# Kernel optimization log

Measured on AMD Instinct MI355X. Metric: run time of the kernel, lower is better.

Reference implementation:

```python
import jax, jax.numpy as jnp
import numpy as np

B = 8; DIM = 384; H = 8; DH = 48; T = 256; T2 = 64; DEPTH = 4; P = 14; G = 16
SCALE = DIM ** -0.5
BN_INV = 1.0 / float(np.sqrt(1.0 + 1e-5))

def _gelu(x):
    return jax.nn.gelu(x, approximate=False)

def _ln(x, g, b):
    m = x.mean(-1, keepdims=True)
    v = ((x - m) ** 2).mean(-1, keepdims=True)
    return (x - m) / jnp.sqrt(v + 1e-5) * g + b

def _conv(x, w, bi, s, p, groups=1):
    y = jax.lax.conv_general_dilated(x, w, (s, s), [(p, p), (p, p)],
        dimension_numbers=('NCHW', 'OIHW', 'NCHW'), feature_group_count=groups)
    return y + bi[None, :, None, None]

def _gumbel_softmax(logits, key, tau=1.0):
    g = jax.random.gumbel(key, logits.shape, logits.dtype)
    return jax.nn.softmax((logits + g) / tau, axis=-1)

def setup_inputs() -> dict:
    key = jax.random.key(0)
    ks = jax.random.split(key, 20)
    def n(k, shape, s=0.02):
        return jax.random.normal(k, shape, jnp.float32) * s
    D = DEPTH
    return {
        'img': jax.random.normal(ks[0], (B, 3, 224, 224), jnp.float32),
        'adj': jax.random.randint(ks[1], (T, T), 0, 2).astype(jnp.int32),
        'ln_g': jnp.ones((D, DIM), jnp.float32), 'ln_b': jnp.zeros((D, DIM), jnp.float32),
        'gcn_wq': n(ks[2], (D, DH, DH)), 'gcn_wk': n(ks[3], (D, DH, DH)), 'gcn_wv': n(ks[4], (D, DH, DH)),
        'wq': n(ks[5], (D, DIM, DIM)), 'wk': n(ks[6], (D, DIM, DIM)), 'wv': n(ks[7], (D, DIM, DIM)),
        'w_kf': n(ks[8], (D, 2 * DIM, H)), 'w_kf2': n(ks[9], (D, H, T)), 'w_kf3': n(ks[10], (D, H, T2)),
        'sD': jnp.ones((D, H, T), jnp.float32), 'sD2': jnp.ones((D, H, T2), jnp.float32),
        'randmat': n(ks[11], (D, H, H), 1.0),
        'conv1_w': n(ks[12], (DIM, 3, 3, 3), 0.05), 'conv1_b': jnp.zeros((DIM,), jnp.float32),
        'bn_g': jnp.ones((DIM,), jnp.float32), 'bn_b': jnp.zeros((DIM,), jnp.float32),
        'conv2_w': n(ks[13], (DIM, 1, 3, 3), 0.05), 'conv2_b': jnp.zeros((DIM,), jnp.float32),
        'emb_w': n(ks[14], (4 * DIM, DIM)), 'emb_b': jnp.zeros((DIM,), jnp.float32),
        'upool_w': n(ks[15], (DIM, T2)), 'upool_b': jnp.zeros((T2,), jnp.float32),
        'upoolout_w': n(ks[16], (DIM, 1)), 'upoolout_b': jnp.zeros((1,), jnp.float32),
    }

def _forward(img, adj, ln_g, ln_b, gcn_wq, gcn_wk, gcn_wv, wq, wk, wv,
             w_kf, w_kf2, w_kf3, sD, sD2, randmat,
             conv1_w, conv1_b, bn_g, bn_b, conv2_w, conv2_b, emb_w, emb_b,
             upool_w, upool_b, upoolout_w, upoolout_b):
    b = img.shape[0]
    # patchify: (b,3,224,224) -> (b*256, 3, 14, 14)
    x = img.reshape(b, 3, G, P, G, P).transpose(0, 2, 4, 1, 3, 5).reshape(b * G * G, 3, P, P)
    y = _conv(x, conv1_w, conv1_b, 2, 1)                       # (b*256,384,7,7)
    y = y * BN_INV * bn_g[None, :, None, None] + bn_b[None, :, None, None]  # BN eval (mean=0,var=1)
    y = _gelu(y)
    y = _conv(y, conv2_w, conv2_b, 2, 1, groups=DIM)           # depthwise -> (b*256,384,4,4)
    y = y.reshape(b * G * G, DIM, 2, 2, 2, 2).max(axis=(3, 5)) # adaptive max pool -> 2x2
    y = y.reshape(b, G * G, DIM * 4)                           # (b,256, c*p1*p2)
    x = y @ emb_w + emb_b                                      # (b,256,384)
    rep_adj = jnp.broadcast_to(adj.astype(jnp.float32)[None, None], (b, H, T, T))

    def attention(xn, adjbh, i, label):
        t = xn.shape[1]
        x4 = xn.reshape(b, t, H, DH).transpose(0, 2, 1, 3)     # b h t d
        q4 = jnp.einsum('bhts,bhsd->bhtd', adjbh, x4 @ gcn_wq[i])  # GCN: A @ (X W)
        k4 = jnp.einsum('bhts,bhsd->bhtd', adjbh, x4 @ gcn_wk[i])
        q = q4.transpose(0, 2, 1, 3).reshape(b, t, DIM) @ wq[i]
        k = k4.transpose(0, 2, 1, 3).reshape(b, t, DIM) @ wk[i]
        rm0 = _gelu(jnp.concatenate([q, k], -1) @ w_kf[i])     # (b,t,h)
        rm = jnp.einsum('bth,btg->bhg', rm0, rm0)
        if label == 0:
            rmd = jax.nn.sigmoid((rm @ w_kf2[i]) / sD[i])      # (b,h,t)
        else:
            rmd = jax.nn.sigmoid((rm @ w_kf3[i]) / sD2[i])
        qh = q.reshape(b, t, H, DH).transpose(0, 2, 1, 3)
        kh = k.reshape(b, t, H, DH).transpose(0, 2, 1, 3)
        score = jnp.einsum('bhld,bhtd->bhlt', qh, kh) * SCALE
        score = jax.nn.leaky_relu(score)
        score = rmd[:, :, :, None] * score * rmd[:, :, None, :]   # diag_embed(rmd) @ S @ diag_embed(rmd)
        score = jnp.einsum('lh,bhk->blk', randmat[i], score.reshape(b, H, t * t)).reshape(b, H, t, t)
        score = jnp.where(adjbh > 0, score, -1e12)
        attn = jax.nn.softmax(score, axis=-1)
        v4 = jnp.einsum('bhts,bhsd->bhtd', attn, x4 @ gcn_wv[i])  # attn weights as edge weights
        return _gelu(v4.transpose(0, 2, 1, 3).reshape(b, t, DIM) @ wv[i])

    kg = jax.random.key(42)
    for i in range(DEPTH):
        xn = _ln(x, ln_g[i], ln_b[i])
        if i < DEPTH // 2:
            x = attention(xn, rep_adj, i, 0) + x
        else:
            if i == DEPTH // 2:
                tmp = (x @ upool_w + upool_b).transpose(0, 2, 1)       # (b,64,256)
                tmp = _gumbel_softmax(tmp, jax.random.fold_in(kg, i))
                x = tmp @ x                                            # (b,64,384)
                rep_adj = jnp.einsum('bls,bhst->bhlt', tmp, rep_adj)   # C A C^T
                rep_adj = jnp.einsum('bhlt,bmt->bhlm', rep_adj, tmp)
                xn = _ln(x, ln_g[i], ln_b[i])
            x = attention(xn, rep_adj, i, 1) + x

    tmp = (x @ upoolout_w + upoolout_b).transpose(0, 2, 1)             # (b,1,64)
    tmp = _gumbel_softmax(tmp, jax.random.fold_in(kg, 99))
    return tmp @ x                                                     # (b,1,384)

def reference(img, adj, ln_g, ln_b, gcn_wq, gcn_wk, gcn_wv, wq, wk, wv,
              w_kf, w_kf2, w_kf3, sD, sD2, randmat,
              conv1_w, conv1_b, bn_g, bn_b, conv2_w, conv2_b, emb_w, emb_b,
              upool_w, upool_b, upoolout_w, upoolout_b):
    return _forward(img, adj, ln_g, ln_b, gcn_wq, gcn_wk, gcn_wv, wq, wk, wv,
                    w_kf, w_kf2, w_kf3, sD, sD2, randmat,
                    conv1_w, conv1_b, bn_g, bn_b, conv2_w, conv2_b, emb_w, emb_b,
                    upool_w, upool_b, upoolout_w, upoolout_b)
```

## Files before the change

### kernel.cpp

```cpp
#include <hip/hip_runtime.h>
#include <stdint.h>
#include <math.h>

#define NB 8
#define NDIM 384
#define NHD 8
#define DHD 48

__device__ float g_patch[2048 * 1536];
__device__ float g_x[NB * 256 * NDIM];
__device__ float g_xb[NB * 64 * NDIM];
__device__ float g_xq[NB * NHD * 256 * DHD];
__device__ float g_xk[NB * NHD * 256 * DHD];
__device__ float g_xv[NB * NHD * 256 * DHD];
__device__ float g_q4[NB * 256 * NDIM];
__device__ float g_k4[NB * 256 * NDIM];
__device__ float g_q[NB * 256 * NDIM];
__device__ float g_k[NB * 256 * NDIM];
__device__ float g_rm0[NB * 256 * NHD];
__device__ float g_rm[NB * 64];
__device__ float g_rmd[NB * NHD * 256];
__device__ float g_score[NB * NHD * 256 * 256];
__device__ float g_score2[NB * NHD * 256 * 256];
__device__ float g_logits[NB * 256 * 64];
__device__ float g_tmp[NB * 64 * 256];
__device__ float g_e1[NB * 64 * 256];
__device__ float g_adj2[NB * 64 * 64];
__device__ float g_lg2[NB * 64];

__device__ __forceinline__ float* dev_buf(int s) {
  switch (s) {
    case 0: return g_patch;
    case 1: return g_x;
    case 2: return g_q4;
    case 3: return g_k4;
    case 4: return g_q;
    case 5: return g_k;
    case 6: return g_logits;
    default: return nullptr;
  }
}
#define SEL_PATCH 0
#define SEL_X 1
#define SEL_Q4 2
#define SEL_K4 3
#define SEL_Q 4
#define SEL_K 5
#define SEL_LOGITS 6

__device__ __forceinline__ float gelu_f(float x) {
  return 0.5f * x * (1.0f + erff(x * 0.70710678118654752440f));
}

__host__ __device__ inline void threefry2x32(uint32_t k0, uint32_t k1,
                                             uint32_t x0, uint32_t x1,
                                             uint32_t* o0, uint32_t* o1) {
  uint32_t ks2 = k0 ^ k1 ^ 0x1BD11BDAu;
#define TF_R(r) { x0 += x1; x1 = (x1 << (r)) | (x1 >> (32 - (r))); x1 ^= x0; }
  x0 += k0; x1 += k1;
  TF_R(13) TF_R(15) TF_R(26) TF_R(6)
  x0 += k1; x1 += ks2 + 1u;
  TF_R(17) TF_R(29) TF_R(16) TF_R(24)
  x0 += ks2; x1 += k0 + 2u;
  TF_R(13) TF_R(15) TF_R(26) TF_R(6)
  x0 += k0; x1 += k1 + 3u;
  TF_R(17) TF_R(29) TF_R(16) TF_R(24)
  x0 += k1; x1 += ks2 + 4u;
  TF_R(13) TF_R(15) TF_R(26) TF_R(6)
  x0 += ks2; x1 += k0 + 5u;
#undef TF_R
  *o0 = x0; *o1 = x1;
}

__device__ __forceinline__ double gumbel_from(uint32_t k0, uint32_t k1,
                                              uint32_t idx) {
  uint32_t o0, o1;
  threefry2x32(k0, k1, 0u, idx, &o0, &o1);
  uint32_t bits = o0 ^ o1;
  uint32_t ub = (bits >> 9) | 0x3f800000u;
  float f = __uint_as_float(ub) - 1.0f;
  const float tiny = 1.17549435e-38f;
  float u = fmaxf(f + tiny, tiny);
  return -log(-log((double)u));
}

__global__ __launch_bounds__(256) void k_patch(const float* __restrict__ img,
                                               const float* __restrict__ w1, const float* __restrict__ b1,
                                               const float* __restrict__ bng, const float* __restrict__ bnb,
                                               const float* __restrict__ w2, const float* __restrict__ b2) {
  __shared__ float s_in[3 * 16 * 16];
  __shared__ float s_c1[96 * 49];
  __shared__ float s_w1[96 * 27];
  const float BN_INV = (float)0.99999500003749968752;
  int p = blockIdx.x;
  int b = p >> 8, g = p & 255, gi = g >> 4, gj = g & 15;
  int tid = threadIdx.x;
  for (int i = tid; i < 3 * 256; i += 256) s_in[i] = 0.f;
  __syncthreads();
  for (int idx = tid; idx < 3 * 196; idx += 256) {
    int c = idx / 196, r = idx % 196, py = r / 14, px = r % 14;
    s_in[c * 256 + (py + 1) * 16 + (px + 1)] =
        img[(((size_t)b * 3 + c) * 224 + gi * 14 + py) * 224 + gj * 14 + px];
  }
  __syncthreads();
  int wave = tid >> 6, lane = tid & 63;
  int y = lane / 7, x = lane - y * 7;
  bool act = lane < 49;
  float in[27];
#pragma unroll
  for (int c = 0; c < 3; ++c)
#pragma unroll
    for (int ky = 0; ky < 3; ++ky)
#pragma unroll
      for (int kx = 0; kx < 3; ++kx)
        in[c * 9 + ky * 3 + kx] = act ? s_in[c * 256 + (2 * y + ky) * 16 + (2 * x + kx)] : 0.f;

  for (int chunk = 0; chunk < 4; ++chunk) {
    int obase = chunk * 96;
    const float4* wsrc = (const float4*)(w1 + obase * 27);
    for (int i = tid; i < 96 * 27 / 4; i += 256) ((float4*)s_w1)[i] = wsrc[i];
    __syncthreads();
    for (int ci = 0; ci < 24; ci += 4) {
      int cl0 = wave * 24 + ci;
      int o0 = obase + cl0;
      float a0 = b1[o0], a1 = b1[o0 + 1], a2 = b1[o0 + 2], a3 = b1[o0 + 3];
      const float* wA = s_w1 + cl0 * 27;
#pragma unroll
      for (int j = 0; j < 27; ++j) {
        float ij = in[j];
        a0 += ij * wA[j];
        a1 += ij * wA[27 + j];
        a2 += ij * wA[54 + j];
        a3 += ij * wA[81 + j];
      }
      a0 = a0 * BN_INV * bng[o0] + bnb[o0];
      a1 = a1 * BN_INV * bng[o0 + 1] + bnb[o0 + 1];
      a2 = a2 * BN_INV * bng[o0 + 2] + bnb[o0 + 2];
      a3 = a3 * BN_INV * bng[o0 + 3] + bnb[o0 + 3];
      if (act) {
        s_c1[cl0 * 49 + lane] = gelu_f(a0);
        s_c1[(cl0 + 1) * 49 + lane] = gelu_f(a1);
        s_c1[(cl0 + 2) * 49 + lane] = gelu_f(a2);
        s_c1[(cl0 + 3) * 49 + lane] = gelu_f(a3);
      }
    }
    __syncthreads();
    if (tid < 96) {
      int cl = tid, c = obase + cl;
      float wd[9];
#pragma unroll
      for (int j = 0; j < 9; ++j) wd[j] = w2[c * 9 + j];
      float bb2 = b2[c];
      const float* sc = &s_c1[cl * 49];
      float o2[4][4];
#pragma unroll
      for (int yy = 0; yy < 4; ++yy)
#pragma unroll
        for (int xx = 0; xx < 4; ++xx) {
          float a = bb2;
#pragma unroll
          for (int ky = 0; ky < 3; ++ky) {
            int iy = 2 * yy + ky - 1;
            if (iy < 0 || iy >= 7) continue;
#pragma unroll
            for (int kx = 0; kx < 3; ++kx) {
              int ix = 2 * xx + kx - 1;
              if (ix < 0 || ix >= 7) continue;
              a += sc[iy * 7 + ix] * wd[ky * 3 + kx];
            }
          }
          o2[yy][xx] = a;
        }
      float4 r;
      r.x = fmaxf(fmaxf(o2[0][0], o2[0][1]), fmaxf(o2[1][0], o2[1][1]));
      r.y = fmaxf(fmaxf(o2[0][2], o2[0][3]), fmaxf(o2[1][2], o2[1][3]));
      r.z = fmaxf(fmaxf(o2[2][0], o2[2][1]), fmaxf(o2[3][0], o2[3][1]));
      r.w = fmaxf(fmaxf(o2[2][2], o2[2][3]), fmaxf(o2[3][2], o2[3][3]));
      *(float4*)&g_patch[(size_t)p * 1536 + c * 4] = r;
    }
    __syncthreads();
  }
}

template <int RPB>
__global__ void k_gemm(const float* __restrict__ W, const float* __restrict__ bias,
                       int selA, int selC, int selR,
                       int M, int K, int N, int act) {
  extern __shared__ float sA[];
  const float* A = dev_buf(selA);
  float* C = dev_buf(selC);
  const float* R = (selR >= 0) ? dev_buf(selR) : nullptr;
  int tid = threadIdx.x;
  int bs = blockDim.x;
  int r0 = blockIdx.x * RPB;
  float acc[RPB];
#pragma unroll
  for (int r = 0; r < RPB; ++r) acc[r] = 0.0f;
  const float4 z4 = {0.f, 0.f, 0.f, 0.f};
  for (int k0 = 0; k0 < K; k0 += 384) {
    __syncthreads();
    for (int idx = tid; idx < RPB * 96; idx += bs) {
      int r = idx / 96, q = idx - r * 96;
      int m = r0 + r;
      ((float4*)sA)[idx] = (m < M) ? ((const float4*)(A + (size_t)m * K + k0))[q] : z4;
    }
    __syncthreads();
    const float* Wp = W + (size_t)k0 * N + tid;
    float w0 = Wp[0], w1 = Wp[N], w2 = Wp[2 * (size_t)N], w3 = Wp[3 * (size_t)N];
#pragma unroll 2
    for (int k = 0; k < 384; k += 4) {
      float n0 = 0.f, n1 = 0.f, n2 = 0.f, n3 = 0.f;
      if (k + 4 < 384) {
        const float* Wn = Wp + (size_t)(k + 4) * N;
        n0 = Wn[0]; n1 = Wn[N]; n2 = Wn[2 * (size_t)N]; n3 = Wn[3 * (size_t)N];
      }
#pragma unroll
      for (int r = 0; r < RPB; ++r) {
        float4 a = *(const float4*)&sA[r * 384 + k];
        acc[r] += a.x * w0 + a.y * w1 + a.z * w2 + a.w * w3;
      }
      w0 = n0; w1 = n1; w2 = n2; w3 = n3;
    }
  }
#pragma unroll
  for (int r = 0; r < RPB; ++r) {
    int m = r0 + r;
    if (m >= M) break;
    float v = acc[r];
    if (bias) v += bias[tid];
    if (act == 1) v = gelu_f(v);
    if (R) v += R[(size_t)m * N + tid];
    C[(size_t)m * N + tid] = v;
  }
}

template <int RPB>
__global__ void k_gemmqk(const float* __restrict__ Wq_, const float* __restrict__ Wk_, int M) {
  __shared__ float sA[RPB * 384];
  int half = gridDim.x >> 1;
  bool isK = blockIdx.x >= half;
  int bid = isK ? blockIdx.x - half : blockIdx.x;
  const float* A = isK ? g_k4 : g_q4;
  float* C = isK ? g_k : g_q;
  const float* W = isK ? Wk_ : Wq_;
  const int N = 384;
  int tid = threadIdx.x;
  int r0 = bid * RPB;
  float acc[RPB];
#pragma unroll
  for (int r = 0; r < RPB; ++r) acc[r] = 0.0f;
  for (int idx = tid; idx < RPB * 96; idx += N) {
    int r = idx / 96, q = idx - r * 96;
    ((float4*)sA)[idx] = ((const float4*)(A + (size_t)(r0 + r) * 384))[q];
  }
  __syncthreads();
  const float* Wp = W + tid;
  float w0 = Wp[0], w1 = Wp[N], w2 = Wp[2 * (size_t)N], w3 = Wp[3 * (size_t)N];
#pragma unroll 2
  for (int k = 0; k < 384; k += 4) {
    float n0 = 0.f, n1 = 0.f, n2 = 0.f, n3 = 0.f;
    if (k + 4 < 384) {
      const float* Wn = Wp + (size_t)(k + 4) * N;
      n0 = Wn[0]; n1 = Wn[N]; n2 = Wn[2 * (size_t)N]; n3 = Wn[3 * (size_t)N];
    }
#pragma unroll
    for (int r = 0; r < RPB; ++r) {
      float4 a = *(const float4*)&sA[r * 384 + k];
      acc[r] += a.x * w0 + a.y * w1 + a.z * w2 + a.w * w3;
    }
    w0 = n0; w1 = n1; w2 = n2; w3 = n3;
  }
#pragma unroll
  for (int r = 0; r < RPB; ++r)
    C[(size_t)(r0 + r) * N + tid] = acc[r];
}

__global__ __launch_bounds__(384) void k_lngcn(const float* __restrict__ gg, const float* __restrict__ bb,
                                               const float* __restrict__ Wq, const float* __restrict__ Wk,
                                               const float* __restrict__ Wv, int t) {
  __shared__ float xn[NDIM];
  __shared__ float wred[6];
  int row = blockIdx.x;
  int b = row / t, tt = row - b * t;
  int tid = threadIdx.x;
  int wid = tid >> 6, lane = tid & 63;
  float v = g_x[(size_t)row * NDIM + tid];
  float s = v;
#pragma unroll
  for (int off = 32; off > 0; off >>= 1) s += __shfl_xor(s, off);
  if (lane == 0) wred[wid] = s;
  __syncthreads();
  float tot = wred[0] + wred[1] + wred[2] + wred[3] + wred[4] + wred[5];
  float mean = tot * (1.0f / 384.0f);
  __syncthreads();
  float d = v - mean;
  s = d * d;
#pragma unroll
  for (int off = 32; off > 0; off >>= 1) s += __shfl_xor(s, off);
  if (lane == 0) wred[wid] = s;
  __syncthreads();
  tot = wred[0] + wred[1] + wred[2] + wred[3] + wred[4] + wred[5];
  float var = tot * (1.0f / 384.0f);
  float inv = 1.0f / sqrtf(var + 1e-5f);
  xn[tid] = d * inv * gg[tid] + bb[tid];
  __syncthreads();
  int h = tid / DHD, dd = tid - h * DHD;
  const float* xh = &xn[h * DHD];
  float aq = 0.f, ak = 0.f, av = 0.f;
#pragma unroll 4
  for (int e = 0; e < DHD; ++e) {
    float xv_ = xh[e];
    aq += xv_ * Wq[e * DHD + dd];
    ak += xv_ * Wk[e * DHD + dd];
    av += xv_ * Wv[e * DHD + dd];
  }
  size_t o = ((size_t)(b * NHD + h) * t + tt) * DHD + dd;
  g_xq[o] = aq; g_xk[o] = ak; g_xv[o] = av;
}

__global__ __launch_bounds__(64) void k_adjmm(const int* __restrict__ adji, int use_adj2, int t) {
  __shared__ float arow[4][256];
  int bid = blockIdx.x;
  int nt = t >> 2;
  int lt = bid % nt; int h = (bid / nt) % NHD; int b = bid / (nt * NHD);
  int l0 = lt * 4;
  int tid = threadIdx.x;
  for (int idx = tid; idx < 4 * t; idx += 64) {
    int r = idx / t, s2 = idx - r * t;
    arow[r][s2] = use_adj2 ? g_adj2[((size_t)b * t + l0 + r) * t + s2]
                           : (float)adji[(l0 + r) * 256 + s2];
  }
  __syncthreads();
  if (tid < DHD) {
    const float* xq = g_xq + (size_t)((b * NHD + h) * t) * DHD + tid;
    const float* xk = g_xk + (size_t)((b * NHD + h) * t) * DHD + tid;
    float aq[4] = {0.f, 0.f, 0.f, 0.f}, ak[4] = {0.f, 0.f, 0.f, 0.f};
    for (int s2 = 0; s2 < t; ++s2) {
      float xqv = xq[(size_t)s2 * DHD];
      float xkv = xk[(size_t)s2 * DHD];
#pragma unroll
      for (int r = 0; r < 4; ++r) {
        aq[r] += arow[r][s2] * xqv;
        ak[r] += arow[r][s2] * xkv;
      }
    }
#pragma unroll
    for (int r = 0; r < 4; ++r) {
      size_t o = ((size_t)b * t + l0 + r) * NDIM + h * DHD + tid;
      g_q4[o] = aq[r]; g_k4[o] = ak[r];
    }
  }
}

__global__ __launch_bounds__(64) void k_kf(const float* __restrict__ Wkf) {
  int row = blockIdx.x;
  int tid = threadIdx.x;
  const float* qrow = g_q + (size_t)row * NDIM;
  const float* krow = g_k + (size_t)row * NDIM;
  float accs[8];
#pragma unroll
  for (int j = 0; j < 8; ++j) accs[j] = 0.f;
  for (int m = tid; m < 768; m += 64) {
    float v = (m < 384) ? qrow[m] : krow[m - 384];
    const float* wr = Wkf + (size_t)m * 8;
#pragma unroll
    for (int j = 0; j < 8; ++j) accs[j] += v * wr[j];
  }
#pragma unroll
  for (int j = 0; j < 8; ++j) {
    float a = accs[j];
    for (int off = 32; off > 0; off >>= 1) a += __shfl_xor(a, off);
    if (tid == 0) g_rm0[(size_t)row * 8 + j] = gelu_f(a);
  }
}

__global__ __launch_bounds__(64) void k_rm(int t) {
  int b = blockIdx.x; int tid = threadIdx.x;
  int h = tid >> 3, g = tid & 7;
  const float* base = g_rm0 + (size_t)b * t * 8;
  float acc = 0.f;
  for (int tt = 0; tt < t; ++tt) acc += base[tt * 8 + h] * base[tt * 8 + g];
  g_rm[b * 64 + tid] = acc;
}

__global__ void k_rmd(const float* __restrict__ Wp, const float* __restrict__ sDp, int t) {
  int id = blockIdx.x * blockDim.x + threadIdx.x;
  int total = NB * NHD * t;
  if (id >= total) return;
  int s = id % t; int h = (id / t) % NHD; int b = id / (t * NHD);
  const float* rm = g_rm + b * 64 + h * 8;
  float acc = 0.f;
#pragma unroll
  for (int g = 0; g < 8; ++g) acc += rm[g] * Wp[g * t + s];
  float val = acc / sDp[h * t + s];
  g_rmd[(size_t)(b * NHD + h) * t + s] = 1.0f / (1.0f + expf(-val));
}

__global__ void k_score(float scale, int t) {
  __shared__ float qs[4][DHD];
  __shared__ float rl[4];
  int bid = blockIdx.x;
  int nt = t >> 2;
  int lt = bid % nt; int h = (bid / nt) % NHD; int b = bid / (nt * NHD);
  int l0 = lt * 4;
  int tid = threadIdx.x;
  for (int idx = tid; idx < 4 * DHD; idx += t) {
    int r = idx / DHD, d = idx - r * DHD;
    qs[r][d] = g_q[((size_t)b * t + l0 + r) * NDIM + h * DHD + d];
  }
  if (tid < 4) rl[tid] = g_rmd[(size_t)(b * NHD + h) * t + l0 + tid];
  __syncthreads();
  const float* krow = g_k + ((size_t)b * t + tid) * NDIM + h * DHD;
  float4 kr[12];
#pragma unroll
  for (int j = 0; j < 12; ++j) kr[j] = *(const float4*)&krow[j * 4];
  float rmd_s = g_rmd[(size_t)(b * NHD + h) * t + tid];
#pragma unroll
  for (int r = 0; r < 4; ++r) {
    float acc = 0.f;
#pragma unroll
    for (int j = 0; j < 12; ++j) {
      float4 qq = *(const float4*)&qs[r][j * 4];
      acc += kr[j].x * qq.x + kr[j].y * qq.y + kr[j].z * qq.z + kr[j].w * qq.w;
    }
    float v = acc * scale;
    v = (v >= 0.f) ? v : 0.01f * v;
    v = rl[r] * v * rmd_s;
    g_score[((size_t)(b * NHD + h) * t + l0 + r) * t + tid] = v;
  }
}

__global__ void k_mixsoft(const float* __restrict__ RM, const int* __restrict__ adji,
                          int use_adj2, int t) {
  extern __shared__ float red2[];
  int bid = blockIdx.x;
  int l = bid % t; int h = (bid / t) % NHD; int b = bid / (t * NHD);
  int tid = threadIdx.x;
  float rm[8];
#pragma unroll
  for (int j = 0; j < 8; ++j) rm[j] = RM[h * 8 + j];
  float acc = 0.f;
#pragma unroll
  for (int j = 0; j < 8; ++j)
    acc += rm[j] * g_score[((size_t)(b * NHD + j) * t + l) * t + tid];
  bool m = use_adj2 ? (g_adj2[((size_t)b * t + l) * t + tid] > 0.f)
                    : (adji[l * 256 + tid] > 0);
  float v = m ? acc : -1e12f;
  red2[tid] = v;
  __syncthreads();
  for (int s = t >> 1; s > 0; s >>= 1) { if (tid < s) red2[tid] = fmaxf(red2[tid], red2[tid + s]); __syncthreads(); }
  float mx = red2[0];
  __syncthreads();
  float e = expf(v - mx);
  red2[tid] = e;
  __syncthreads();
  for (int s = t >> 1; s > 0; s >>= 1) { if (tid < s) red2[tid] += red2[tid + s]; __syncthreads(); }
  g_score2[((size_t)(b * NHD + h) * t + l) * t + tid] = e / red2[0];
}

__global__ __launch_bounds__(64) void k_attnv(int t) {
  __shared__ float arow[4][256];
  int bid = blockIdx.x;
  int nt = t >> 2;
  int lt = bid % nt; int h = (bid / nt) % NHD; int b = bid / (nt * NHD);
  int l0 = lt * 4;
  int tid = threadIdx.x;
  for (int idx = tid; idx < 4 * t; idx += 64) {
    int r = idx / t, s2 = idx - r * t;
    arow[r][s2] = g_score2[((size_t)(b * NHD + h) * t + l0 + r) * t + s2];
  }
  __syncthreads();
  if (tid < DHD) {
    const float* xv = g_xv + (size_t)((b * NHD + h) * t) * DHD + tid;
    float acc[4] = {0.f, 0.f, 0.f, 0.f};
    for (int s2 = 0; s2 < t; ++s2) {
      float xvv = xv[(size_t)s2 * DHD];
#pragma unroll
      for (int r = 0; r < 4; ++r) acc[r] += arow[r][s2] * xvv;
    }
#pragma unroll
    for (int r = 0; r < 4; ++r)
      g_q4[((size_t)b * t + l0 + r) * NDIM + h * DHD + tid] = acc[r];
  }
}

__global__ __launch_bounds__(256) void k_gumbel_pool(uint32_t k0, uint32_t k1) {
  __shared__ double red2[256];
  int bj = blockIdx.x;
  int b = bj >> 6, j = bj & 63;
  int tt = threadIdx.x;
  uint32_t n = (uint32_t)bj * 256u + (uint32_t)tt;
  double gum = gumbel_from(k0, k1, n);
  double val = (double)g_logits[((size_t)b * 256 + tt) * 64 + j] + gum;
  red2[tt] = val; __syncthreads();
  for (int s = 128; s > 0; s >>= 1) { if (tt < s) red2[tt] = fmax(red2[tt], red2[tt + s]); __syncthreads(); }
  double mx = red2[0]; __syncthreads();
  double e = exp(val - mx);
  red2[tt] = e; __syncthreads();
  for (int s = 128; s > 0; s >>= 1) { if (tt < s) red2[tt] += red2[tt + s]; __syncthreads(); }
  g_tmp[(size_t)bj * 256 + tt] = (float)(e / red2[0]);
}

__global__ __launch_bounds__(384) void k_poolx() {
  __shared__ float trow[256];
  int bj = blockIdx.x; int b = bj >> 6;
  int tid = threadIdx.x;
  if (tid < 256) trow[tid] = g_tmp[(size_t)bj * 256 + tid];
  __syncthreads();
  float acc = 0.f;
  const float* xb = g_x + (size_t)b * 256 * NDIM + tid;
  for (int tt = 0; tt < 256; ++tt) acc += trow[tt] * xb[(size_t)tt * NDIM];
  g_xb[(size_t)bj * NDIM + tid] = acc;
}

__global__ void k_copyx(int n) {
  int i = blockIdx.x * blockDim.x + threadIdx.x;
  if (i < n) g_x[i] = g_xb[i];
}

__global__ __launch_bounds__(256) void k_pooladj1(const int* __restrict__ adji) {
  __shared__ float trow[256];
  int bl = blockIdx.x;
  int tid = threadIdx.x;
  trow[tid] = g_tmp[(size_t)bl * 256 + tid];
  __syncthreads();
  float acc = 0.f;
  for (int s = 0; s < 256; ++s) acc += trow[s] * (float)adji[s * 256 + tid];
  g_e1[(size_t)bl * 256 + tid] = acc;
}

__global__ __launch_bounds__(64) void k_pooladj2() {
  __shared__ float erow[256];
  int bl = blockIdx.x; int b = bl >> 6;
  int tid = threadIdx.x;
  for (int s = tid; s < 256; s += 64) erow[s] = g_e1[(size_t)bl * 256 + s];
  __syncthreads();
  const float* tm = g_tmp + ((size_t)b * 64 + tid) * 256;
  float acc = 0.f;
  for (int s = 0; s < 256; ++s) acc += erow[s] * tm[s];
  g_adj2[(size_t)bl * 64 + tid] = acc;
}

__global__ __launch_bounds__(64) void k_outlogits(const float* __restrict__ w, const float* __restrict__ bias) {
  int row = blockIdx.x;
  int tid = threadIdx.x;
  const float* x = g_x + (size_t)row * NDIM;
  float acc = 0.f;
  for (int c = tid; c < NDIM; c += 64) acc += x[c] * w[c];
  for (int off = 32; off > 0; off >>= 1) acc += __shfl_xor(acc, off);
  if (tid == 0) g_lg2[row] = acc + bias[0];
}

__global__ __launch_bounds__(384) void k_final(uint32_t k0, uint32_t k1, float* __restrict__ out) {
  __shared__ double sv[64];
  __shared__ double sp[64];
  int b = blockIdx.x;
  int tid = threadIdx.x;
  if (tid < 64) {
    uint32_t n = (uint32_t)(b * 64 + tid);
    sv[tid] = (double)g_lg2[b * 64 + tid] + gumbel_from(k0, k1, n);
  }
  __syncthreads();
  double mx = -1e30;
  for (int i2 = 0; i2 < 64; ++i2) mx = fmax(mx, sv[i2]);
  if (tid < 64) sp[tid] = exp(sv[tid] - mx);
  __syncthreads();
  double sum = 0.;
  for (int i2 = 0; i2 < 64; ++i2) sum += sp[i2];
  float acc = 0.f;
  const float* xb = g_x + (size_t)b * 64 * NDIM + tid;
  for (int tt = 0; tt < 64; ++tt) acc += (float)(sp[tt] / sum) * xb[(size_t)tt * NDIM];
  out[(size_t)b * NDIM + tid] = acc;
}

extern "C" void kernel_launch(void* const* d_in, const int* in_sizes, int n_in,
                              void* d_out, int out_size, void* d_ws, size_t ws_size,
                              hipStream_t stream) {
  const float* img = (const float*)d_in[0];
  const int* adj = (const int*)d_in[1];
  const float* ln_g = (const float*)d_in[2];
  const float* ln_b = (const float*)d_in[3];
  const float* gcn_wq = (const float*)d_in[4];
  const float* gcn_wk = (const float*)d_in[5];
  const float* gcn_wv = (const float*)d_in[6];
  const float* wq = (const float*)d_in[7];
  const float* wk = (const float*)d_in[8];
  const float* wv = (const float*)d_in[9];
  const float* w_kf = (const float*)d_in[10];
  const float* w_kf2 = (const float*)d_in[11];
  const float* w_kf3 = (const float*)d_in[12];
  const float* sD = (const float*)d_in[13];
  const float* sD2 = (const float*)d_in[14];
  const float* randmat = (const float*)d_in[15];
  const float* conv1_w = (const float*)d_in[16];
  const float* conv1_b = (const float*)d_in[17];
  const float* bn_g = (const float*)d_in[18];
  const float* bn_b = (const float*)d_in[19];
  const float* conv2_w = (const float*)d_in[20];
  const float* conv2_b = (const float*)d_in[21];
  const float* emb_w = (const float*)d_in[22];
  const float* emb_b = (const float*)d_in[23];
  const float* upool_w = (const float*)d_in[24];
  const float* upool_b = (const float*)d_in[25];
  const float* upoolout_w = (const float*)d_in[26];
  const float* upoolout_b = (const float*)d_in[27];
  float* out = (float*)d_out;

  uint32_t k2a, k2b, k99a, k99b;
  threefry2x32(0u, 42u, 0u, 2u, &k2a, &k2b);
  threefry2x32(0u, 42u, 0u, 99u, &k99a, &k99b);

  const float SCALE = (float)(1.0 / sqrt(384.0));

  k_patch<<<2048, 256, 0, stream>>>(img, conv1_w, conv1_b, bn_g, bn_b, conv2_w, conv2_b);
  k_gemm<8><<<256, 384, 8 * 384 * sizeof(float), stream>>>(
      emb_w, emb_b, SEL_PATCH, SEL_X, -1, 2048, 1536, 384, 0);

  auto attention = [&](int i, int t, int label) {
    int rows = NB * t;
    int bht = NB * NHD * t;
    int bht4 = bht / 4;
    int use_adj2 = (t == 64) ? 1 : 0;
    k_lngcn<<<rows, 384, 0, stream>>>(ln_g + i * 384, ln_b + i * 384,
                                      gcn_wq + i * 2304, gcn_wk + i * 2304,
                                      gcn_wv + i * 2304, t);
    k_adjmm<<<bht4, 64, 0, stream>>>(adj, use_adj2, t);
    if (rows == 2048) {
      k_gemmqk<4><<<1024, 384, 0, stream>>>(wq + i * 147456, wk + i * 147456, rows);
    } else {
      k_gemmqk<2><<<512, 384, 0, stream>>>(wq + i * 147456, wk + i * 147456, rows);
    }
    k_kf<<<rows, 64, 0, stream>>>(w_kf + i * 6144);
    k_rm<<<NB, 64, 0, stream>>>(t);
    const float* Wp = label ? (w_kf3 + i * 512) : (w_kf2 + i * 2048);
    const float* sDp = label ? (sD2 + i * 512) : (sD + i * 2048);
    int totr = NB * NHD * t;
    k_rmd<<<(totr + 255) / 256, 256, 0, stream>>>(Wp, sDp, t);
    k_score<<<bht4, t, 0, stream>>>(SCALE, t);
    k_mixsoft<<<bht, t, t * sizeof(float), stream>>>(randmat + i * 64, adj, use_adj2, t);
    k_attnv<<<bht4, 64, 0, stream>>>(t);
    if (rows == 2048) {
      k_gemm<4><<<512, 384, 4 * 384 * sizeof(float), stream>>>(
          wv + i * 147456, nullptr, SEL_Q4, SEL_X, SEL_X, rows, 384, 384, 1);
    } else {
      k_gemm<2><<<256, 384, 2 * 384 * sizeof(float), stream>>>(
          wv + i * 147456, nullptr, SEL_Q4, SEL_X, SEL_X, rows, 384, 384, 1);
    }
  };

  attention(0, 256, 0);
  attention(1, 256, 0);

  k_gemm<2><<<1024, 64, 2 * 384 * sizeof(float), stream>>>(
      upool_w, upool_b, SEL_X, SEL_LOGITS, -1, 2048, 384, 64, 0);
  k_gumbel_pool<<<512, 256, 0, stream>>>(k2a, k2b);
  k_poolx<<<512, 384, 0, stream>>>();
  k_copyx<<<(NB * 64 * NDIM + 255) / 256, 256, 0, stream>>>(NB * 64 * NDIM);
  k_pooladj1<<<512, 256, 0, stream>>>(adj);
  k_pooladj2<<<512, 64, 0, stream>>>();

  attention(2, 64, 1);
  attention(3, 64, 1);

  k_outlogits<<<512, 64, 0, stream>>>(upoolout_w, upoolout_b);
  k_final<<<8, 384, 0, stream>>>(k99a, k99b, out);
}
```

Measured before the change: 1.082 ms.

## Split patch conv per channel chunk, split-K embedding GEMM, widen rm reduction

The patch kernel now launches one block per (patch, 96-channel chunk) rather than looping over four chunks inside a block. This gives four times more blocks and drops the per-chunk barriers, at the cost of recomputing the input tile load in each block. The embedding GEMM is split along K into four 384-wide slices, with partial results written to the score scratch buffer and summed plus bias by a separate reduction kernel. This raises parallelism from 256 blocks to 1024, in exchange for extra global traffic and a launch. k_rm now uses 256 threads that split the t-loop four ways and reduce through shared memory.

New measurement: 925.5 us. 14.5% less time.

```diff
diff --git a/kernel.cpp b/kernel.cpp
--- a/kernel.cpp
+++ b/kernel.cpp
@@ -92,16 +92,20 @@
   __shared__ float s_c1[96 * 49];
   __shared__ float s_w1[96 * 27];
   const float BN_INV = (float)0.99999500003749968752;
-  int p = blockIdx.x;
+  int p = blockIdx.x >> 2;
+  int chunk = blockIdx.x & 3;
+  int obase = chunk * 96;
   int b = p >> 8, g = p & 255, gi = g >> 4, gj = g & 15;
   int tid = threadIdx.x;
-  for (int i = tid; i < 3 * 256; i += 256) s_in[i] = 0.f;
-  __syncthreads();
-  for (int idx = tid; idx < 3 * 196; idx += 256) {
-    int c = idx / 196, r = idx % 196, py = r / 14, px = r % 14;
-    s_in[c * 256 + (py + 1) * 16 + (px + 1)] =
-        img[(((size_t)b * 3 + c) * 224 + gi * 14 + py) * 224 + gj * 14 + px];
-  }
+  for (int idx = tid; idx < 3 * 256; idx += 256) {
+    int c = idx >> 8, r = idx & 255, py = r >> 4, px = r & 15;
+    float v = 0.f;
+    if (py >= 1 && py <= 14 && px >= 1 && px <= 14)
+      v = img[(((size_t)b * 3 + c) * 224 + gi * 14 + py - 1) * 224 + gj * 14 + px - 1];
+    s_in[idx] = v;
+  }
+  const float4* wsrc = (const float4*)(w1 + obase * 27);
+  for (int i = tid; i < 96 * 27 / 4; i += 256) ((float4*)s_w1)[i] = wsrc[i];
   __syncthreads();
   int wave = tid >> 6, lane = tid & 63;
   int y = lane / 7, x = lane - y * 7;
@@ -115,70 +119,63 @@
       for (int kx = 0; kx < 3; ++kx)
         in[c * 9 + ky * 3 + kx] = act ? s_in[c * 256 + (2 * y + ky) * 16 + (2 * x + kx)] : 0.f;
 
-  for (int chunk = 0; chunk < 4; ++chunk) {
-    int obase = chunk * 96;
-    const float4* wsrc = (const float4*)(w1 + obase * 27);
-    for (int i = tid; i < 96 * 27 / 4; i += 256) ((float4*)s_w1)[i] = wsrc[i];
-    __syncthreads();
-    for (int ci = 0; ci < 24; ci += 4) {
-      int cl0 = wave * 24 + ci;
-      int o0 = obase + cl0;
-      float a0 = b1[o0], a1 = b1[o0 + 1], a2 = b1[o0 + 2], a3 = b1[o0 + 3];
-      const float* wA = s_w1 + cl0 * 27;
-#pragma unroll
-      for (int j = 0; j < 27; ++j) {
-        float ij = in[j];
-        a0 += ij * wA[j];
-        a1 += ij * wA[27 + j];
-        a2 += ij * wA[54 + j];
-        a3 += ij * wA[81 + j];
+  for (int ci = 0; ci < 24; ci += 4) {
+    int cl0 = wave * 24 + ci;
+    int o0 = obase + cl0;
+    float a0 = b1[o0], a1 = b1[o0 + 1], a2 = b1[o0 + 2], a3 = b1[o0 + 3];
+    const float* wA = s_w1 + cl0 * 27;
+#pragma unroll
+    for (int j = 0; j < 27; ++j) {
+      float ij = in[j];
+      a0 += ij * wA[j];
+      a1 += ij * wA[27 + j];
+      a2 += ij * wA[54 + j];
+      a3 += ij * wA[81 + j];
+    }
+    a0 = a0 * BN_INV * bng[o0] + bnb[o0];
+    a1 = a1 * BN_INV * bng[o0 + 1] + bnb[o0 + 1];
+    a2 = a2 * BN_INV * bng[o0 + 2] + bnb[o0 + 2];
+    a3 = a3 * BN_INV * bng[o0 + 3] + bnb[o0 + 3];
+    if (act) {
+      s_c1[cl0 * 49 + lane] = gelu_f(a0);
+      s_c1[(cl0 + 1) * 49 + lane] = gelu_f(a1);
+      s_c1[(cl0 + 2) * 49 + lane] = gelu_f(a2);
+      s_c1[(cl0 + 3) * 49 + lane] = gelu_f(a3);
+    }
+  }
+  __syncthreads();
+  if (tid < 96) {
+    int cl = tid, c = obase + cl;
+    float wd[9];
+#pragma unroll
+    for (int j = 0; j < 9; ++j) wd[j] = w2[c * 9 + j];
+    float bb2 = b2[c];
+    const float* sc = &s_c1[cl * 49];
+    float o2[4][4];
+#pragma unroll
+    for (int yy = 0; yy < 4; ++yy)
+#pragma unroll
+      for (int xx = 0; xx < 4; ++xx) {
+        float a = bb2;
+#pragma unroll
+        for (int ky = 0; ky < 3; ++ky) {
+          int iy = 2 * yy + ky - 1;
+          if (iy < 0 || iy >= 7) continue;
+#pragma unroll
+          for (int kx = 0; kx < 3; ++kx) {
+            int ix = 2 * xx + kx - 1;
+            if (ix < 0 || ix >= 7) continue;
+            a += sc[iy * 7 + ix] * wd[ky * 3 + kx];
+          }
+        }
+        o2[yy][xx] = a;
       }
-      a0 = a0 * BN_INV * bng[o0] + bnb[o0];
-      a1 = a1 * BN_INV * bng[o0 + 1] + bnb[o0 + 1];
-      a2 = a2 * BN_INV * bng[o0 + 2] + bnb[o0 + 2];
-      a3 = a3 * BN_INV * bng[o0 + 3] + bnb[o0 + 3];
-      if (act) {
-        s_c1[cl0 * 49 + lane] = gelu_f(a0);
-        s_c1[(cl0 + 1) * 49 + lane] = gelu_f(a1);
-        s_c1[(cl0 + 2) * 49 + lane] = gelu_f(a2);
-        s_c1[(cl0 + 3) * 49 + lane] = gelu_f(a3);
-      }
-    }
-    __syncthreads();
-    if (tid < 96) {
-      int cl = tid, c = obase + cl;
-      float wd[9];
-#pragma unroll
-      for (int j = 0; j < 9; ++j) wd[j] = w2[c * 9 + j];
-      float bb2 = b2[c];
-      const float* sc = &s_c1[cl * 49];
-      float o2[4][4];
-#pragma unroll
-      for (int yy = 0; yy < 4; ++yy)
-#pragma unroll
-        for (int xx = 0; xx < 4; ++xx) {
-          float a = bb2;
-#pragma unroll
-          for (int ky = 0; ky < 3; ++ky) {
-            int iy = 2 * yy + ky - 1;
-            if (iy < 0 || iy >= 7) continue;
-#pragma unroll
-            for (int kx = 0; kx < 3; ++kx) {
-              int ix = 2 * xx + kx - 1;
-              if (ix < 0 || ix >= 7) continue;
-              a += sc[iy * 7 + ix] * wd[ky * 3 + kx];
-            }
-          }
-          o2[yy][xx] = a;
-        }
-      float4 r;
-      r.x = fmaxf(fmaxf(o2[0][0], o2[0][1]), fmaxf(o2[1][0], o2[1][1]));
-      r.y = fmaxf(fmaxf(o2[0][2], o2[0][3]), fmaxf(o2[1][2], o2[1][3]));
-      r.z = fmaxf(fmaxf(o2[2][0], o2[2][1]), fmaxf(o2[3][0], o2[3][1]));
-      r.w = fmaxf(fmaxf(o2[2][2], o2[2][3]), fmaxf(o2[3][2], o2[3][3]));
-      *(float4*)&g_patch[(size_t)p * 1536 + c * 4] = r;
-    }
-    __syncthreads();
+    float4 r;
+    r.x = fmaxf(fmaxf(o2[0][0], o2[0][1]), fmaxf(o2[1][0], o2[1][1]));
+    r.y = fmaxf(fmaxf(o2[0][2], o2[0][3]), fmaxf(o2[1][2], o2[1][3]));
+    r.z = fmaxf(fmaxf(o2[2][0], o2[2][1]), fmaxf(o2[3][0], o2[3][1]));
+    r.w = fmaxf(fmaxf(o2[2][2], o2[2][3]), fmaxf(o2[3][2], o2[3][3]));
+    *(float4*)&g_patch[(size_t)p * 1536 + c * 4] = r;
   }
 }
 
@@ -234,6 +231,52 @@
   }
 }
 
+__global__ __launch_bounds__(384) void k_gemm_sk(const float* __restrict__ W, int M, int K, int N) {
+  __shared__ float sA[8 * 384];
+  int mb = M >> 3;
+  int kc = blockIdx.x / mb;
+  int rb = blockIdx.x - kc * mb;
+  int r0 = rb << 3;
+  int k0 = kc * 384;
+  int tid = threadIdx.x;
+  float acc[8];
+#pragma unroll
+  for (int r = 0; r < 8; ++r) acc[r] = 0.0f;
+  for (int idx = tid; idx < 8 * 96; idx += 384) {
+    int r = idx / 96, q = idx - r * 96;
+    ((float4*)sA)[idx] = ((const float4*)(g_patch + (size_t)(r0 + r) * K + k0))[q];
+  }
+  __syncthreads();
+  const float* Wp = W + (size_t)k0 * N + tid;
+  float w0 = Wp[0], w1 = Wp[N], w2 = Wp[2 * (size_t)N], w3 = Wp[3 * (size_t)N];
+#pragma unroll 2
+  for (int k = 0; k < 384; k += 4) {
+    float n0 = 0.f, n1 = 0.f, n2 = 0.f, n3 = 0.f;
+    if (k + 4 < 384) {
+      const float* Wn = Wp + (size_t)(k + 4) * N;
+      n0 = Wn[0]; n1 = Wn[N]; n2 = Wn[2 * (size_t)N]; n3 = Wn[3 * (size_t)N];
+    }
+#pragma unroll
+    for (int r = 0; r < 8; ++r) {
+      float4 a = *(const float4*)&sA[r * 384 + k];
+      acc[r] += a.x * w0 + a.y * w1 + a.z * w2 + a.w * w3;
+    }
+    w0 = n0; w1 = n1; w2 = n2; w3 = n3;
+  }
+#pragma unroll
+  for (int r = 0; r < 8; ++r)
+    g_score[((size_t)kc * M + r0 + r) * N + tid] = acc[r];
+}
+
+__global__ void k_gemm_skred(const float* __restrict__ bias, int M, int N) {
+  int i = blockIdx.x * blockDim.x + threadIdx.x;
+  int total = M * N;
+  if (i >= total) return;
+  size_t stride = (size_t)M * N;
+  float v = g_score[i] + g_score[i + stride] + g_score[i + 2 * stride] + g_score[i + 3 * stride];
+  g_x[i] = v + bias[i % N];
+}
+
 template <int RPB>
 __global__ void k_gemmqk(const float* __restrict__ Wq_, const float* __restrict__ Wk_, int M) {
   __shared__ float sA[RPB * 384];
@@ -374,13 +417,19 @@
   }
 }
 
-__global__ __launch_bounds__(64) void k_rm(int t) {
+__global__ __launch_bounds__(256) void k_rm(int t) {
+  __shared__ float red[256];
   int b = blockIdx.x; int tid = threadIdx.x;
-  int h = tid >> 3, g = tid & 7;
-  const float* base = g_rm0 + (size_t)b * t * 8;
+  int out = tid & 63, slice = tid >> 6;
+  int h = out >> 3, g = out & 7;
+  int t4 = t >> 2;
+  const float* base = g_rm0 + (size_t)b * t * 8 + (size_t)slice * t4 * 8;
   float acc = 0.f;
-  for (int tt = 0; tt < t; ++tt) acc += base[tt * 8 + h] * base[tt * 8 + g];
-  g_rm[b * 64 + tid] = acc;
+  for (int tt = 0; tt < t4; ++tt) acc += base[tt * 8 + h] * base[tt * 8 + g];
+  red[slice * 64 + out] = acc;
+  __syncthreads();
+  if (tid < 64)
+    g_rm[b * 64 + tid] = red[tid] + red[64 + tid] + red[128 + tid] + red[192 + tid];
 }
 
 __global__ void k_rmd(const float* __restrict__ Wp, const float* __restrict__ sDp, int t) {
@@ -612,9 +661,9 @@
 
   const float SCALE = (float)(1.0 / sqrt(384.0));
 
-  k_patch<<<2048, 256, 0, stream>>>(img, conv1_w, conv1_b, bn_g, bn_b, conv2_w, conv2_b);
-  k_gemm<8><<<256, 384, 8 * 384 * sizeof(float), stream>>>(
-      emb_w, emb_b, SEL_PATCH, SEL_X, -1, 2048, 1536, 384, 0);
+  k_patch<<<2048 * 4, 256, 0, stream>>>(img, conv1_w, conv1_b, bn_g, bn_b, conv2_w, conv2_b);
+  k_gemm_sk<<<1024, 384, 0, stream>>>(emb_w, 2048, 1536, 384);
+  k_gemm_skred<<<(2048 * 384 + 255) / 256, 256, 0, stream>>>(emb_b, 2048, 384);
 
   auto attention = [&](int i, int t, int label) {
     int rows = NB * t;
@@ -631,7 +680,7 @@
       k_gemmqk<2><<<512, 384, 0, stream>>>(wq + i * 147456, wk + i * 147456, rows);
     }
     k_kf<<<rows, 64, 0, stream>>>(w_kf + i * 6144);
-    k_rm<<<NB, 64, 0, stream>>>(t);
+    k_rm<<<NB, 256, 0, stream>>>(t);
     const float* Wp = label ? (w_kf3 + i * 512) : (w_kf2 + i * 2048);
     const float* sDp = label ? (sD2 + i * 512) : (sD + i * 2048);
     int totr = NB * NHD * t;
```
